# Kernel optimization log

Hardware: AMD Instinct MI355X
Metric: run time of the kernel (lower is better)

The kernel has to match this reference:

```python
import jax, jax.numpy as jnp
import numpy as np

N_ITER = 4
D = 768  # word_emb_dim == sent_dim of both CrossAttentionBlocks


def setup_inputs() -> dict:
    key = jax.random.key(0)
    ks = jax.random.split(key, 6)
    N_S, N_F = 16384, 4096
    return {
        "sents_emb": jax.random.normal(ks[0], (N_S, D), jnp.float32),
        "func_embed": jax.random.normal(ks[1], (N_F, D), jnp.float32),
        "Wv_f2s": jax.random.normal(ks[2], (D, D), jnp.float32) * 0.02,
        "bv_f2s": jax.random.normal(ks[3], (D,), jnp.float32) * 0.02,
        "Wv_s2f": jax.random.normal(ks[4], (D, D), jnp.float32) * 0.02,
        "bv_s2f": jax.random.normal(ks[5], (D,), jnp.float32) * 0.02,
    }


def reference(sents_emb, func_embed, Wv_f2s, bv_f2s, Wv_s2f, bv_s2f):
    scale = 1.0 / jnp.sqrt(jnp.asarray(D, sents_emb.dtype))
    sents_hid, func_hid = sents_emb, func_embed
    z = None
    for _ in range(N_ITER):  # small fixed iteration count, sequential dependency
        # func2sent: query=sents_hid, key=func_hid, value=W_v(func_hid)
        func_val = func_hid @ Wv_f2s.T + bv_f2s              # [N_f, D]
        z = scale * (sents_hid @ func_hid.T)                  # [N_s, N_f] logits (returned)
        att = jax.nn.softmax(z, axis=1)
        sents_hid = sents_hid + att @ func_val                # [N_s, D]
        # sent2func: query=func_hid, key=sents_hid, value=W_v(sents_hid)
        sent_val = sents_hid @ Wv_s2f.T + bv_s2f              # [N_s, D]
        z2 = scale * (func_hid @ sents_hid.T)                 # [N_f, N_s]
        func_hid = func_hid + jax.nn.softmax(z2, axis=1) @ sent_val
    return (sents_hid, func_hid, z)
```

## Files before the change

### kernel.cpp

```cpp
#include <hip/hip_runtime.h>
#include <stdint.h>

typedef __attribute__((ext_vector_type(8))) short s16x8;
typedef __attribute__((ext_vector_type(8))) unsigned short u16x8;
typedef __attribute__((ext_vector_type(4))) unsigned short u16x4;
typedef __attribute__((ext_vector_type(4))) float f32x4;

__device__ inline unsigned short f2b(float f){
  unsigned u = __builtin_bit_cast(unsigned, f);
  u = u + 0x7fffu + ((u >> 16) & 1u);
  return (unsigned short)(u >> 16);
}
__device__ inline float b2f(unsigned short h){
  unsigned u = ((unsigned)h) << 16;
  return __builtin_bit_cast(float, u);
}

typedef __attribute__((address_space(1))) const unsigned g_uint;
typedef __attribute__((address_space(3))) unsigned l_uint;

__device__ inline void gload_lds16(const void* g, void* l){
  __builtin_amdgcn_global_load_lds((g_uint*)reinterpret_cast<uintptr_t>(g),
                                   (l_uint*)reinterpret_cast<uintptr_t>(l), 16, 0, 0);
}

template<int EPI>
__global__ __launch_bounds__(256, 4) void gemm_bt(
    const unsigned short* __restrict__ A, const unsigned short* __restrict__ B,
    int M, int N, int KS, float scale, const float* __restrict__ bias,
    const float* __restrict__ linv,
    float* __restrict__ Cf, unsigned short* __restrict__ Cb)
{
  __shared__ unsigned short As[128*64];
  __shared__ unsigned short Bs[128*64];
  const int tid  = threadIdx.x;
  const int wid  = tid >> 6, lane = tid & 63;
  const int wr   = wid >> 1, wc = wid & 1;

  const unsigned gx = gridDim.x, gy = gridDim.y;
  const unsigned lin = blockIdx.x + gx*(blockIdx.y + gy*blockIdx.z);
  const unsigned q   = (gx*gy*gridDim.z) >> 3;
  const unsigned w   = (lin & 7)*q + (lin >> 3);
  const unsigned bxs = w % gx;
  const unsigned rest = w / gx;
  const unsigned bys = rest % gy;
  const unsigned bzs = rest / gy;

  const int bm   = bys * 128, bn = bxs * 128;
  const int kb   = bzs * KS, ke = kb + KS;

  f32x4 acc[4][4] = {};

  const int l8   = lane >> 3;
  const int scol = ((((lane & 7) << 4) ^ (l8 << 4)) >> 1);
  const int Klead = gridDim.z * KS;

  const unsigned short* Ag[4]; const unsigned short* Bg[4];
  unsigned short* Al[4]; unsigned short* Bl[4];
  #pragma unroll
  for (int i = 0; i < 4; ++i){
    const int row = wid*32 + i*8 + l8;
    Ag[i] = A + (size_t)(bm + row) * Klead + scol;
    Bg[i] = B + (size_t)(bn + row) * Klead + scol;
    Al[i] = As + (wid*4 + i) * 512;
    Bl[i] = Bs + (wid*4 + i) * 512;
  }

  const int fr    = lane & 15;
  const int fk    = (lane >> 4) << 4;
  const int amask = (fr & 7) << 4;

  for (int k0 = kb; k0 < ke; k0 += 64){
    if (k0 != kb) __syncthreads();
    #pragma unroll
    for (int i = 0; i < 4; ++i){
      gload_lds16(Ag[i] + k0, Al[i]);
      gload_lds16(Bg[i] + k0, Bl[i]);
    }
    __syncthreads();
    #pragma unroll
    for (int kk = 0; kk < 2; ++kk){
      s16x8 af[4], bf[4];
      #pragma unroll
      for (int m = 0; m < 4; ++m){
        const int row = (wr << 6) + m*16 + fr;
        const int off = row*128 + (((kk << 6) + fk) ^ amask);
        af[m] = *(const s16x8*)((const char*)As + off);
      }
      #pragma unroll
      for (int n = 0; n < 4; ++n){
        const int row = (wc << 6) + n*16 + fr;
        const int off = row*128 + (((kk << 6) + fk) ^ amask);
        bf[n] = *(const s16x8*)((const char*)Bs + off);
      }
      #pragma unroll
      for (int m = 0; m < 4; ++m)
        #pragma unroll
        for (int n = 0; n < 4; ++n)
          acc[m][n] = __builtin_amdgcn_mfma_f32_16x16x32_bf16(af[m], bf[n], acc[m][n], 0, 0, 0);
    }
  }

  const int gr0 = bm + (wr << 6) + ((lane >> 4) << 2);
  const int gc0 = bn + (wc << 6) + (lane & 15);
  const size_t pbase = (size_t)bzs * M * N;
  #pragma unroll
  for (int m = 0; m < 4; ++m){
    #pragma unroll
    for (int j = 0; j < 4; ++j){
      const int row = gr0 + m*16 + j;
      const float li = (EPI == 7) ? linv[row] : 0.f;
      #pragma unroll
      for (int n = 0; n < 4; ++n){
        const int col = gc0 + n*16;
        const size_t idx = (size_t)row * N + col;
        const float v = acc[m][n][j];
        if      (EPI == 2) Cb[idx] = f2b(v + bias[row]);
        else if (EPI == 4) Cf[pbase + idx] = v;
        else if (EPI == 5) Cb[idx] = f2b(__expf(v * scale));
        else if (EPI == 6){ const float zz = v * scale; Cf[idx] = zz; Cb[idx] = f2b(__expf(zz)); }
        else if (EPI == 7){ const float o = Cf[idx] + li * v; Cf[idx] = o; Cb[idx] = f2b(o); }
      }
    }
  }
}

__global__ __launch_bounds__(256) void rowsum_att(const unsigned short* __restrict__ E,
                                                  int C, float* __restrict__ linv)
{
  const int row = blockIdx.x, t = threadIdx.x;
  const int lane = t & 63, wid = t >> 6;
  __shared__ float red[4];
  const u16x8* p = (const u16x8*)(E + (size_t)row * C) + t;
  const int nc = C >> 11;
  float s = 0.f;
  for (int c = 0; c < nc; ++c){
    const u16x8 a = p[c * 256];
    #pragma unroll
    for (int j = 0; j < 8; ++j) s += b2f(a[j]);
  }
  #pragma unroll
  for (int o = 32; o; o >>= 1) s += __shfl_xor(s, o, 64);
  if (lane == 0) red[wid] = s;
  __syncthreads();
  if (t == 0) linv[row] = 1.0f / (red[0] + red[1] + red[2] + red[3]);
}

__global__ __launch_bounds__(256) void reduce_splitk(
    const float* __restrict__ P, int S, size_t stride4,
    const float* __restrict__ linv, int d4,
    float* __restrict__ Cf, unsigned short* __restrict__ Cb, int n4)
{
  const int i = blockIdx.x * 256 + threadIdx.x;
  if (i >= n4) return;
  f32x4 s = {0.f, 0.f, 0.f, 0.f};
  for (int k = 0; k < S; ++k) s += ((const f32x4*)P)[(size_t)k * stride4 + i];
  const float li = linv[i / d4];
  f32x4 r = ((const f32x4*)Cf)[i];
  r += s * li;
  ((f32x4*)Cf)[i] = r;
  u16x4 o;
  o[0] = f2b(r[0]); o[1] = f2b(r[1]); o[2] = f2b(r[2]); o[3] = f2b(r[3]);
  ((u16x4*)Cb)[i] = o;
}

__global__ void cvt8(const float* __restrict__ src, float* __restrict__ dstf,
                     unsigned short* __restrict__ dstb, int n8)
{
  const int i = blockIdx.x * 256 + threadIdx.x;
  if (i >= n8) return;
  const f32x4 a = ((const f32x4*)src)[2*i];
  const f32x4 b = ((const f32x4*)src)[2*i + 1];
  if (dstf){ ((f32x4*)dstf)[2*i] = a; ((f32x4*)dstf)[2*i + 1] = b; }
  u16x8 o;
  o[0]=f2b(a[0]); o[1]=f2b(a[1]); o[2]=f2b(a[2]); o[3]=f2b(a[3]);
  o[4]=f2b(b[0]); o[5]=f2b(b[1]); o[6]=f2b(b[2]); o[7]=f2b(b[3]);
  ((u16x8*)dstb)[i] = o;
}

extern "C" void kernel_launch(void* const* d_in, const int* in_sizes, int n_in,
                              void* d_out, int out_size, void* d_ws, size_t ws_size,
                              hipStream_t stream)
{
  (void)in_sizes; (void)n_in; (void)out_size; (void)ws_size;
  const float* sents = (const float*)d_in[0];
  const float* funcs = (const float*)d_in[1];
  const float* WvA   = (const float*)d_in[2];
  const float* bvA   = (const float*)d_in[3];
  const float* WvB   = (const float*)d_in[4];
  const float* bvB   = (const float*)d_in[5];

  const int NS = 16384, NF = 4096, D = 768;

  float* outS = (float*)d_out;
  float* outF = outS + (size_t)NS * D;
  float* outZ = outF + (size_t)NF * D;

  char* ws = (char*)d_ws;
  unsigned short* att = (unsigned short*)ws;  ws += (size_t)NS * NF * 2;
  unsigned short* z2  = att;
  unsigned short* sb  = (unsigned short*)ws;  ws += (size_t)NS * D * 2;
  unsigned short* fb  = (unsigned short*)ws;  ws += (size_t)NF * D * 2;
  unsigned short* fvT = (unsigned short*)ws;  ws += (size_t)D * NF * 2;
  unsigned short* svT = (unsigned short*)ws;  ws += (size_t)D * NS * 2;
  unsigned short* wA  = (unsigned short*)ws;  ws += (size_t)D * D * 2;
  unsigned short* wB  = (unsigned short*)ws;  ws += (size_t)D * D * 2;
  float* linv = (float*)ws;  ws += (size_t)NS * 4;
  float* Pbuf = (float*)ws;  ws += (size_t)NF * D * 4 * 4;

  const float scale = 0.036084391824351615f;

  cvt8<<<dim3((NS*D/8 + 255)/256), 256, 0, stream>>>(sents, outS, sb, NS*D/8);
  cvt8<<<dim3((NF*D/8 + 255)/256), 256, 0, stream>>>(funcs, outF, fb, NF*D/8);
  cvt8<<<dim3((D*D/8 + 255)/256),  256, 0, stream>>>(WvA, nullptr, wA, D*D/8);
  cvt8<<<dim3((D*D/8 + 255)/256),  256, 0, stream>>>(WvB, nullptr, wB, D*D/8);

  for (int it = 0; it < 4; ++it){
    gemm_bt<2><<<dim3(NF/128, D/128, 1), dim3(256), 0, stream>>>(wA, fb, D, NF, D, 0.f, bvA, nullptr, nullptr, fvT);
    if (it < 3){
      gemm_bt<5><<<dim3(NF/128, NS/128, 1), dim3(256), 0, stream>>>(sb, fb, NS, NF, D, scale, nullptr, nullptr, nullptr, att);
    } else {
      gemm_bt<6><<<dim3(NF/128, NS/128, 1), dim3(256), 0, stream>>>(sb, fb, NS, NF, D, scale, nullptr, nullptr, outZ, att);
    }
    rowsum_att<<<dim3(NS), 256, 0, stream>>>(att, NF, linv);
    gemm_bt<7><<<dim3(D/128, NS/128, 1), dim3(256), 0, stream>>>(att, fvT, NS, D, NF, 0.f, nullptr, linv, outS, sb);
    gemm_bt<2><<<dim3(NS/128, D/128, 1), dim3(256), 0, stream>>>(wB, sb, D, NS, D, 0.f, bvB, nullptr, nullptr, svT);
    gemm_bt<5><<<dim3(NS/128, NF/128, 1), dim3(256), 0, stream>>>(fb, sb, NF, NS, D, scale, nullptr, nullptr, nullptr, z2);
    rowsum_att<<<dim3(NF), 256, 0, stream>>>(z2, NS, linv);
    gemm_bt<4><<<dim3(D/128, NF/128, 4), dim3(256), 0, stream>>>(z2, svT, NF, D, 4096, 0.f, nullptr, nullptr, Pbuf, nullptr);
    reduce_splitk<<<dim3(NF*D/4/256), 256, 0, stream>>>(Pbuf, 4, (size_t)NF*D/4, linv, D/4, outF, fb, NF*D/4);
  }
}
```

Baseline: 2.425 ms.

## Add 256x256-tile 512-thread GEMM with interleaved async LDS staging for logits

Introduces a new gemm256 kernel with 256x256 output tiles, 8 waves, double-buffered LDS (128KB) filled by global_load_lds, XOR-swizzled layouts, and fine-grained interleaving of half-tile loads with MFMA phases using setprio. It replaces the 128x128 gemm_bt for the two big logit/exp GEMMs (sents x funcs and funcs x sents). The larger tile raises arithmetic intensity and cuts global traffic per FLOP. In exchange it adds many more barriers, high register pressure from 128 accumulators per thread, and lower occupancy.

```diff
diff --git a/kernel.cpp b/kernel.cpp
--- a/kernel.cpp
+++ b/kernel.cpp
@@ -22,6 +22,148 @@
 __device__ inline void gload_lds16(const void* g, void* l){
   __builtin_amdgcn_global_load_lds((g_uint*)reinterpret_cast<uintptr_t>(g),
                                    (l_uint*)reinterpret_cast<uintptr_t>(l), 16, 0, 0);
+}
+
+#define BARF() { __builtin_amdgcn_s_barrier(); asm volatile("" ::: "memory"); }
+
+template<int EPI>
+__global__ __launch_bounds__(512, 2) void gemm256(
+    const unsigned short* __restrict__ A, const unsigned short* __restrict__ B,
+    int M, int N, int K, float scale,
+    float* __restrict__ Cf, unsigned short* __restrict__ Cb)
+{
+  __shared__ __align__(16) char ldsraw[131072];
+  const int tid  = threadIdx.x;
+  const int wid  = tid >> 6, lane = tid & 63;
+  const int wm   = wid >> 2, wn = wid & 3;
+
+  const unsigned gx = gridDim.x, gy = gridDim.y;
+  const unsigned lin = blockIdx.x + gx*blockIdx.y;
+  const unsigned q   = (gx*gy) >> 3;
+  const unsigned w   = (lin & 7)*q + (lin >> 3);
+  const int bm = (w / gx) * 256, bn = (w % gx) * 256;
+
+  const int NT = K >> 6;
+
+  f32x4 acc[8][4] = {};
+
+  auto stageA = [&](int T, int halfm){
+    const int kb = T << 6;
+    char* ldsb = ldsraw + ((T & 1) << 16) + halfm*16384;
+    #pragma unroll
+    for (int i = 0; i < 2; ++i){
+      const int lr  = i*64 + (tid >> 3);
+      const int gtr = halfm*64 + ((lr < 64) ? lr : lr + 64);
+      const int sc  = ((tid & 7)*8) ^ ((lr & 7)*8);
+      gload_lds16(A + (size_t)(bm + gtr)*K + kb + sc, ldsb + i*8192 + tid*16);
+    }
+  };
+  auto stageB = [&](int T, int halfk){
+    const int kb = (T << 6) + halfk*32;
+    char* ldsb = ldsraw + ((T & 1) << 16) + 32768 + halfk*16384;
+    #pragma unroll
+    for (int i = 0; i < 2; ++i){
+      const int lr = i*128 + (tid >> 2);
+      const int sc = ((tid & 3)*8) ^ ((lr & 3)*8);
+      gload_lds16(B + (size_t)(bn + lr)*K + kb + sc, ldsb + i*8192 + tid*16);
+    }
+  };
+
+  const int fr = lane & 15;
+  const int fo = (lane >> 4) << 4;
+  const int amask = (fr & 7) << 4;
+  const int bmask = (fr & 3) << 4;
+
+  auto rdA = [&](const char* ldsS, int mh, int kk, s16x8* af){
+    const char* ab = ldsS + mh*16384;
+    #pragma unroll
+    for (int mf = 0; mf < 4; ++mf){
+      const int r = wm*64 + mf*16 + fr;
+      af[mf] = *(const s16x8*)(ab + r*128 + ((kk*64 + fo) ^ amask));
+    }
+  };
+  auto rdB = [&](const char* ldsS, int kk, s16x8* bf){
+    const char* bb = ldsS + 32768 + kk*16384;
+    #pragma unroll
+    for (int nf = 0; nf < 4; ++nf){
+      const int r = wn*64 + nf*16 + fr;
+      bf[nf] = *(const s16x8*)(bb + r*64 + (fo ^ bmask));
+    }
+  };
+
+  stageB(0, 0); stageA(0, 0); stageA(0, 1); stageB(0, 1);
+  stageB(1, 0); stageA(1, 0);
+  asm volatile("s_waitcnt vmcnt(4)" ::: "memory");
+  BARF();
+
+  for (int T = 0; T < NT; ++T){
+    const char* ldsS = ldsraw + ((T & 1) << 16);
+    s16x8 af[4], bf[4];
+    rdA(ldsS, 0, 0, af); rdB(ldsS, 0, bf);
+    if (T + 1 < NT) stageA(T + 1, 1);
+    BARF();
+    __builtin_amdgcn_s_setprio(1);
+    #pragma unroll
+    for (int mf = 0; mf < 4; ++mf)
+      #pragma unroll
+      for (int nf = 0; nf < 4; ++nf)
+        acc[mf][nf] = __builtin_amdgcn_mfma_f32_16x16x32_bf16(af[mf], bf[nf], acc[mf][nf], 0, 0, 0);
+    __builtin_amdgcn_s_setprio(0);
+    BARF();
+    rdA(ldsS, 1, 0, af);
+    if (T + 1 < NT) stageB(T + 1, 1);
+    BARF();
+    __builtin_amdgcn_s_setprio(1);
+    #pragma unroll
+    for (int mf = 0; mf < 4; ++mf)
+      #pragma unroll
+      for (int nf = 0; nf < 4; ++nf)
+        acc[4 + mf][nf] = __builtin_amdgcn_mfma_f32_16x16x32_bf16(af[mf], bf[nf], acc[4 + mf][nf], 0, 0, 0);
+    __builtin_amdgcn_s_setprio(0);
+    BARF();
+    rdA(ldsS, 0, 1, af); rdB(ldsS, 1, bf);
+    if (T + 2 < NT) stageB(T + 2, 0);
+    BARF();
+    __builtin_amdgcn_s_setprio(1);
+    #pragma unroll
+    for (int mf = 0; mf < 4; ++mf)
+      #pragma unroll
+      for (int nf = 0; nf < 4; ++nf)
+        acc[mf][nf] = __builtin_amdgcn_mfma_f32_16x16x32_bf16(af[mf], bf[nf], acc[mf][nf], 0, 0, 0);
+    __builtin_amdgcn_s_setprio(0);
+    BARF();
+    rdA(ldsS, 1, 1, af);
+    if (T + 2 < NT) stageA(T + 2, 0);
+    BARF();
+    __builtin_amdgcn_s_setprio(1);
+    #pragma unroll
+    for (int mf = 0; mf < 4; ++mf)
+      #pragma unroll
+      for (int nf = 0; nf < 4; ++nf)
+        acc[4 + mf][nf] = __builtin_amdgcn_mfma_f32_16x16x32_bf16(af[mf], bf[nf], acc[4 + mf][nf], 0, 0, 0);
+    __builtin_amdgcn_s_setprio(0);
+    if (T < NT - 2) { asm volatile("s_waitcnt vmcnt(4)" ::: "memory"); }
+    else           { asm volatile("s_waitcnt vmcnt(0)" ::: "memory"); }
+    BARF();
+  }
+
+  const int er0 = bm + wm*128 + ((lane >> 4) << 2);
+  const int ec0 = bn + wn*64  + (lane & 15);
+  #pragma unroll
+  for (int mf = 0; mf < 8; ++mf){
+    #pragma unroll
+    for (int nf = 0; nf < 4; ++nf){
+      #pragma unroll
+      for (int j = 0; j < 4; ++j){
+        const int row = er0 + mf*16 + j;
+        const int col = ec0 + nf*16;
+        const size_t idx = (size_t)row * N + col;
+        const float v = acc[mf][nf][j];
+        if (EPI == 5) Cb[idx] = f2b(__expf(v * scale));
+        else { const float zz = v * scale; Cf[idx] = zz; Cb[idx] = f2b(__expf(zz)); }
+      }
+    }
+  }
 }
 
 template<int EPI>
@@ -117,8 +259,6 @@
         const float v = acc[m][n][j];
         if      (EPI == 2) Cb[idx] = f2b(v + bias[row]);
         else if (EPI == 4) Cf[pbase + idx] = v;
-        else if (EPI == 5) Cb[idx] = f2b(__expf(v * scale));
-        else if (EPI == 6){ const float zz = v * scale; Cf[idx] = zz; Cb[idx] = f2b(__expf(zz)); }
         else if (EPI == 7){ const float o = Cf[idx] + li * v; Cf[idx] = o; Cb[idx] = f2b(o); }
       }
     }
@@ -218,14 +358,14 @@
   for (int it = 0; it < 4; ++it){
     gemm_bt<2><<<dim3(NF/128, D/128, 1), dim3(256), 0, stream>>>(wA, fb, D, NF, D, 0.f, bvA, nullptr, nullptr, fvT);
     if (it < 3){
-      gemm_bt<5><<<dim3(NF/128, NS/128, 1), dim3(256), 0, stream>>>(sb, fb, NS, NF, D, scale, nullptr, nullptr, nullptr, att);
+      gemm256<5><<<dim3(NF/256, NS/256), dim3(512), 0, stream>>>(sb, fb, NS, NF, D, scale, nullptr, att);
     } else {
-      gemm_bt<6><<<dim3(NF/128, NS/128, 1), dim3(256), 0, stream>>>(sb, fb, NS, NF, D, scale, nullptr, nullptr, outZ, att);
+      gemm256<6><<<dim3(NF/256, NS/256), dim3(512), 0, stream>>>(sb, fb, NS, NF, D, scale, outZ, att);
     }
     rowsum_att<<<dim3(NS), 256, 0, stream>>>(att, NF, linv);
     gemm_bt<7><<<dim3(D/128, NS/128, 1), dim3(256), 0, stream>>>(att, fvT, NS, D, NF, 0.f, nullptr, linv, outS, sb);
     gemm_bt<2><<<dim3(NS/128, D/128, 1), dim3(256), 0, stream>>>(wB, sb, D, NS, D, 0.f, bvB, nullptr, nullptr, svT);
-    gemm_bt<5><<<dim3(NS/128, NF/128, 1), dim3(256), 0, stream>>>(fb, sb, NF, NS, D, scale, nullptr, nullptr, nullptr, z2);
+    gemm256<5><<<dim3(NS/256, NF/256), dim3(512), 0, stream>>>(fb, sb, NF, NS, D, scale, nullptr, z2);
     rowsum_att<<<dim3(NF), 256, 0, stream>>>(z2, NS, linv);
     gemm_bt<4><<<dim3(D/128, NF/128, 4), dim3(256), 0, stream>>>(z2, svT, NF, D, 4096, 0.f, nullptr, nullptr, Pbuf, nullptr);
     reduce_splitk<<<dim3(NF*D/4/256), 256, 0, stream>>>(Pbuf, 4, (size_t)NF*D/4, linv, D/4, outF, fb, NF*D/4);
```

New measurement: 2.269 ms. 6.4% less time.
